# Optimization experiments

Hardware: AMD Instinct MI355X
Metric: run time of the kernel (lower is better)

The kernel has to match this reference:

```python
import jax, jax.numpy as jnp
import numpy as np
from jax import lax

NUM_HEADS = 4
KEY_DEPTHS = 32
ATTN_CH = 32
OUT_CH = 64
IN_CH = 32
KSIZE = 3


def circ_conv3d(x, w, b=None):
    # x: (B,C,D,H,W), w: (O,I,k,k,k); circular padding keeps spatial dims.
    k = w.shape[-1]
    p = k // 2
    if p > 0:
        x = jnp.pad(x, ((0, 0), (0, 0), (p, p), (p, p), (p, p)), mode='wrap')
    y = lax.conv_general_dilated(x, w, (1, 1, 1), 'VALID',
                                 dimension_numbers=('NCDHW', 'OIDHW', 'NCDHW'))
    if b is not None:
        y = y + b[None, :, None, None, None]
    return y


def setup_inputs() -> dict:
    key = jax.random.key(0)
    k1, k2, k3, k4, k5 = jax.random.split(key, 5)
    x = jax.random.normal(k1, (2, IN_CH, 16, 16, 16), dtype=jnp.float32)
    fan = IN_CH * KSIZE ** 3
    w_init = jax.random.normal(k2, (OUT_CH - ATTN_CH, IN_CH, KSIZE, KSIZE, KSIZE), dtype=jnp.float32) / np.sqrt(fan)
    w_qkv = jax.random.normal(k3, (2 * KEY_DEPTHS + ATTN_CH, IN_CH, KSIZE, KSIZE, KSIZE), dtype=jnp.float32) / np.sqrt(fan)
    w_out = jax.random.normal(k4, (ATTN_CH, ATTN_CH, 1, 1, 1), dtype=jnp.float32) / np.sqrt(ATTN_CH)
    b_out = jax.random.normal(k5, (ATTN_CH,), dtype=jnp.float32) * 0.01
    return {'x': x, 'w_init': w_init, 'w_qkv': w_qkv, 'w_out': w_out, 'b_out': b_out}


def reference(x, w_init, w_qkv, w_out, b_out):
    out = circ_conv3d(x, w_init)                      # (b, out-attn, w,h,d)
    b, _, w, h, d = out.shape
    qkv = circ_conv3d(x, w_qkv)                       # (b, 2dk+dv, w,h,d)
    q, k, v = jnp.split(qkv, [KEY_DEPTHS, 2 * KEY_DEPTHS], axis=1)
    dk_h = KEY_DEPTHS // NUM_HEADS
    dv_h = ATTN_CH // NUM_HEADS
    N = w * h * d
    scale = dk_h ** -0.5
    fq = q.reshape(b, NUM_HEADS, dk_h, N) * scale     # (b,H,dk_h,N)
    fk = k.reshape(b, NUM_HEADS, dk_h, N)
    fv = v.reshape(b, NUM_HEADS, dv_h, N)
    logits = jnp.einsum('bhcn,bhcm->bhnm', fq, fk)    # (b,H,N,N)
    weights = jax.nn.softmax(logits, axis=-1)
    attn = jnp.einsum('bhnm,bhvm->bhnv', weights, fv)  # (b,H,N,dv_h)
    # Faithful to torch: a pure reshape (memory reinterpretation), not a transpose.
    attn = attn.reshape(b, NUM_HEADS, dv_h, w, h, d)
    attn = attn.reshape(b, NUM_HEADS * dv_h, w, h, d)  # combine heads
    attn = circ_conv3d(attn, w_out, b_out)             # 1x1x1 conv
    return jnp.concatenate([out, attn], axis=1)
```

## Files before the change

### kernel.cpp

```cpp
#include <hip/hip_runtime.h>


typedef short short8 __attribute__((ext_vector_type(8)));
typedef float float4v __attribute__((ext_vector_type(4)));
typedef unsigned short ushort_t;
typedef unsigned int uint_t;

__device__ inline ushort_t f2bf(float x) {
  uint_t u = __builtin_bit_cast(uint_t, x);
  u += 0x7FFFu + ((u >> 16) & 1u);
  return (ushort_t)(u >> 16);
}

__device__ inline uint_t cvtpk(float lo, float hi) {
  uint_t r;
  asm("v_cvt_pk_bf16_f32 %0, %1, %2" : "=v"(r) : "v"(lo), "v"(hi));
  return r;
}

__global__ __launch_bounds__(256) void kPrep(const float* __restrict__ w_init,
                                             const float* __restrict__ w_qkv,
                                             const float* __restrict__ x,
                                             ushort_t* __restrict__ wA,
                                             ushort_t* __restrict__ xb) {
  __shared__ float xsf[256 * 34];
  int t = threadIdx.x;
  int bx = blockIdx.x;
  if (bx < 432) {
    int idx = bx * 256 + t;
    int j = idx & 7;
    int lane = (idx >> 3) & 63;
    int tap = (idx >> 9) % 27;
    int otile = idx / (27 * 512);
    int o = otile * 16 + (lane & 15);
    int ic = (lane >> 4) * 8 + j;
    const float QS = 0.35355339059327373f * 1.4426950408889634f;
    float v;
    if (o < 32) v = w_init[(o * 32 + ic) * 27 + tap];
    else        v = w_qkv[((o - 32) * 32 + ic) * 27 + tap];
    if (o >= 32 && o < 64) v *= QS;
    wA[idx] = f2bf(v);
  } else {
    int bxx = bx - 432;
    int z = bxx & 15, b = bxx >> 4;
#pragma unroll
    for (int ic = 0; ic < 32; ++ic)
      xsf[t * 34 + ic] = x[((size_t)(b * 32 + ic) * 16 + z) * 256 + t];
    __syncthreads();
#pragma unroll
    for (int r = 0; r < 4; ++r) {
      int slot = r * 256 + t;
      int s = slot >> 2;
      int icg = slot & 3;
      ushort_t tmp[8];
#pragma unroll
      for (int jj = 0; jj < 8; ++jj) tmp[jj] = f2bf(xsf[s * 34 + icg * 8 + jj]);
      *(short8*)(xb + ((size_t)(b * 16 + z) * 256 + s) * 32 + icg * 8) = *(short8*)tmp;
    }
  }
}

__global__ __launch_bounds__(256, 1) void kConv(const ushort_t* __restrict__ xb,
                                                const ushort_t* __restrict__ wA,
                                                float* __restrict__ out,
                                                ushort_t* __restrict__ Qbf,
                                                ushort_t* __restrict__ Kbf,
                                                ushort_t* __restrict__ VtTp) {
  __shared__ ushort_t xs[3 * 256 * 32];
  int tid = threadIdx.x;
  int w = tid >> 6, lane = tid & 63;
  int quad = lane >> 4, nl = lane & 15;
  int bx = blockIdx.x;
  int oq = bx & 3;
  int z = (bx >> 2) & 15;
  int b = bx >> 6;

#pragma unroll
  for (int j = 0; j < 12; ++j) {
    int idx = j * 256 + tid;
    int p = idx >> 10;
    int rem = idx & 1023;
    int zr = (z + p + 15) & 15;
    *(short8*)(xs + p * 8192 + rem * 8) =
        *(const short8*)(xb + (size_t)(b * 16 + zr) * 8192 + rem * 8);
  }
  __syncthreads();

  float4v acc[2][4];
#pragma unroll
  for (int ot = 0; ot < 2; ++ot)
#pragma unroll
    for (int st = 0; st < 4; ++st) acc[ot][st] = (float4v){0.f, 0.f, 0.f, 0.f};

  int y0 = w * 4;
  for (int tap = 0; tap < 27; ++tap) {
    int kz = tap / 9, kyx = tap % 9;
    int ky = kyx / 3, kx = kyx % 3;
    short8 afrag[2];
#pragma unroll
    for (int ot = 0; ot < 2; ++ot)
      afrag[ot] = *(const short8*)(wA + ((size_t)((oq * 2 + ot) * 27 + tap) * 64 + lane) * 8);
    int xsh = (nl + kx + 15) & 15;
#pragma unroll
    for (int st = 0; st < 4; ++st) {
      int yy = (y0 + st + ky + 15) & 15;
      short8 bfrag = *(const short8*)(xs + ((kz * 256) + yy * 16 + xsh) * 32 + quad * 8);
#pragma unroll
      for (int ot = 0; ot < 2; ++ot)
        acc[ot][st] = __builtin_amdgcn_mfma_f32_16x16x32_bf16(afrag[ot], bfrag, acc[ot][st], 0, 0, 0);
    }
  }

#pragma unroll
  for (int st = 0; st < 4; ++st) {
    int y = y0 + st;
    int s = z * 256 + y * 16 + nl;
    int mperm = 2 * nl + (y & 1);
#pragma unroll
    for (int ot = 0; ot < 2; ++ot) {
      int otg = oq * 2 + ot;
#pragma unroll
      for (int r = 0; r < 4; ++r) {
        float val = acc[ot][st][r];
        int oo = (otg & 1) * 16 + quad * 4 + r;
        if (otg < 2) {
          out[(size_t)(b * 64 + oo) * 4096 + s] = val;
        } else if (otg < 4) {
          int h = oo >> 3, c = oo & 7;
          Qbf[((size_t)(b * 4 + h) * 4096 + s) * 8 + c] = f2bf(val);
        } else if (otg < 6) {
          int h = oo >> 3, c = oo & 7;
          Kbf[((size_t)(b * 4 + h) * 4096 + s) * 8 + c] = f2bf(val);
        } else {
          int h = oo >> 3, c = oo & 7;
          VtTp[((size_t)(b * 4 + h) * 8 + c) * 4096 + (size_t)(s & ~31) + mperm] = f2bf(val);
        }
      }
    }
  }
}

__global__ __launch_bounds__(256) void kAttn(const ushort_t* __restrict__ Qbf,
                                             const ushort_t* __restrict__ Kbf,
                                             const ushort_t* __restrict__ VtTp,
                                             float* __restrict__ pacc,
                                             float* __restrict__ pl) {
  __shared__ ushort_t Plds[4 * 2 * 16 * 40];
  int tid = threadIdx.x;
  int w = tid >> 6, lane = tid & 63;
  int id = blockIdx.x * 4 + w;
  int bh = id >> 10;
  int ksp = (id >> 8) & 3;
  int ntile = id & 255;
  int n0 = ntile * 16;
  int quad = lane >> 4, nl = lane & 15;
  int v = nl;

  short8 aq = {};
  if (quad == 0) aq = *(const short8*)(Qbf + ((size_t)bh * 4096 + n0 + nl) * 8);

  short8 ones8;
#pragma unroll
  for (int i = 0; i < 8; ++i) ones8[i] = (short)0x3F80;

  const ushort_t* Krows = Kbf + ((size_t)bh * 4096 + ksp * 1024) * 8;
  const ushort_t* Vbase = VtTp + ((size_t)bh * 8 + (v < 8 ? v : 0)) * 4096
                          + ksp * 1024 + quad * 8;
  ushort_t* Pw = Plds + w * 2 * 640;
  uint_t* Pw32 = (uint_t*)Pw;

  float4v acc = {};

#define QKEXP(mi)                                                              \
  {                                                                            \
    int m0 = (mi) * 32;                                                        \
    short8 bk0 = {}, bk1 = {};                                                 \
    if (quad == 0) {                                                           \
      bk0 = *(const short8*)(Krows + (size_t)(m0 + nl) * 8);                   \
      bk1 = *(const short8*)(Krows + (size_t)(m0 + 16 + nl) * 8);              \
    }                                                                          \
    float4v s0 = __builtin_amdgcn_mfma_f32_16x16x32_bf16(                      \
        aq, bk0, (float4v){0.f, 0.f, 0.f, 0.f}, 0, 0, 0);                      \
    float4v s1 = __builtin_amdgcn_mfma_f32_16x16x32_bf16(                      \
        aq, bk1, (float4v){0.f, 0.f, 0.f, 0.f}, 0, 0, 0);                      \
    uint_t* Pt32 = Pw32 + ((mi) & 1) * 320;                                    \
    _Pragma("unroll") for (int r = 0; r < 4; ++r) {                            \
      float e0 = __builtin_amdgcn_exp2f(s0[r]);                                \
      float e1 = __builtin_amdgcn_exp2f(s1[r]);                                \
      Pt32[(quad * 4 + r) * 20 + nl] = cvtpk(e0, e1);                          \
    }                                                                          \
  }

#define PV(mi)                                                                 \
  {                                                                            \
    const ushort_t* Pt = Pw + ((mi) & 1) * 640;                                \
    short8 a2 = *(const short8*)(Pt + nl * 40 + quad * 8);                     \
    short8 b2;                                                                 \
    if (v < 8)       b2 = *(const short8*)(Vbase + (mi) * 32);                 \
    else if (v == 8) b2 = ones8;                                               \
    else             b2 = (short8){};                                          \
    acc = __builtin_amdgcn_mfma_f32_16x16x32_bf16(a2, b2, acc, 0, 0, 0);       \
  }

  QKEXP(0)
#pragma unroll 2
  for (int mi = 1; mi < 32; ++mi) {
    QKEXP(mi)
    PV(mi - 1)
  }
  PV(31)
#undef QKEXP
#undef PV

#pragma unroll
  for (int r = 0; r < 4; ++r) {
    int rowg = bh * 4096 + n0 + quad * 4 + r;
    if (v < 8)       pacc[((size_t)rowg * 4 + ksp) * 8 + v] = acc[r];
    else if (v == 8) pl[(size_t)rowg * 4 + ksp] = acc[r];
  }
}

__global__ __launch_bounds__(256) void kMerge(const float* __restrict__ pacc,
                                              const float* __restrict__ pl,
                                              float* __restrict__ attn) {
  int idx = blockIdx.x * 256 + threadIdx.x;
  int row = idx >> 3;
  int c = idx & 7;
  float l = 0.f, a = 0.f;
#pragma unroll
  for (int s = 0; s < 4; ++s) {
    l += pl[(size_t)row * 4 + s];
    a += pacc[((size_t)row * 4 + s) * 8 + c];
  }
  int b = row >> 14;
  int h = (row >> 12) & 3;
  int n = row & 4095;
  attn[((size_t)(b * 32 + h * 8 + (n >> 9)) << 12) + ((n & 511) * 8 + c)] = a / l;
}

__global__ __launch_bounds__(256) void kOut(const float* __restrict__ attn,
                                            const float* __restrict__ w_out,
                                            const float* __restrict__ b_out,
                                            float* __restrict__ out) {
  int idx = blockIdx.x * 256 + threadIdx.x;
  int s = idx & 4095;
  int b = (idx >> 12) & 1;
  int cp = idx >> 13;
  float a[32];
#pragma unroll
  for (int ci = 0; ci < 32; ++ci) a[ci] = attn[(size_t)(b * 32 + ci) * 4096 + s];
#pragma unroll
  for (int oo = 0; oo < 2; ++oo) {
    int co = cp * 2 + oo;
    float r = b_out[co];
#pragma unroll
    for (int ci = 0; ci < 32; ++ci) r = fmaf(w_out[co * 32 + ci], a[ci], r);
    out[(size_t)(b * 64 + 32 + co) * 4096 + s] = r;
  }
}

extern "C" void kernel_launch(void* const* d_in, const int* in_sizes, int n_in,
                              void* d_out, int out_size, void* d_ws, size_t ws_size,
                              hipStream_t stream) {
  const float* x      = (const float*)d_in[0];
  const float* w_init = (const float*)d_in[1];
  const float* w_qkv  = (const float*)d_in[2];
  const float* w_out  = (const float*)d_in[3];
  const float* b_out  = (const float*)d_in[4];
  float* out = (float*)d_out;

  ushort_t* wA  = (ushort_t*)d_ws;
  ushort_t* xb  = wA + 110592;
  ushort_t* Qbf = xb + 262144;
  ushort_t* Kbf = Qbf + 262144;
  ushort_t* VtTp = Kbf + 262144;
  float* attn = (float*)(VtTp + 262144);
  float* pacc = attn + 262144;
  float* pl = pacc + 1048576;

  kPrep <<<464,  256, 0, stream>>>(w_init, w_qkv, x, wA, xb);
  kConv <<<128,  256, 0, stream>>>(xb, wA, out, Qbf, Kbf, VtTp);
  kAttn <<<2048, 256, 0, stream>>>(Qbf, Kbf, VtTp, pacc, pl);
  kMerge<<<1024, 256, 0, stream>>>(pacc, pl, attn);
  kOut  <<<512,  256, 0, stream>>>(attn, w_out, b_out, out);
}
```

Before: 124.0 us.

## Process two query tiles per wave in attention, sharing K and V loads

Each wave now handles 32 query rows (two 16-row tiles) instead of 16, so every loaded K block and V block serves both tiles and the grid is halved. The K operand is loaded by all 32 lanes, with the query placed in quad 0 or quad 1 to select the key half, and the next K block is prefetched a step ahead. This cuts redundant global K/V traffic and per-wave overhead. In exchange it uses more registers and LDS per wave and launches half as many waves, which can reduce occupancy and latency hiding.

```diff
diff --git a/kernel.cpp b/kernel.cpp
--- a/kernel.cpp
+++ b/kernel.cpp
@@ -145,78 +145,103 @@
                                              const ushort_t* __restrict__ VtTp,
                                              float* __restrict__ pacc,
                                              float* __restrict__ pl) {
-  __shared__ ushort_t Plds[4 * 2 * 16 * 40];
+  __shared__ ushort_t Plds[4 * 2 * 2 * 640];
   int tid = threadIdx.x;
   int w = tid >> 6, lane = tid & 63;
   int id = blockIdx.x * 4 + w;
-  int bh = id >> 10;
-  int ksp = (id >> 8) & 3;
-  int ntile = id & 255;
-  int n0 = ntile * 16;
+  int bh = id >> 9;
+  int ksp = (id >> 7) & 3;
+  int ntile = id & 127;
+  int n0 = ntile * 32;
   int quad = lane >> 4, nl = lane & 15;
+  int l31 = lane & 31;
   int v = nl;
 
-  short8 aq = {};
-  if (quad == 0) aq = *(const short8*)(Qbf + ((size_t)bh * 4096 + n0 + nl) * 8);
+  short8 z8 = {};
+  short8 q0f = *(const short8*)(Qbf + ((size_t)bh * 4096 + n0 + nl) * 8);
+  short8 q1f = *(const short8*)(Qbf + ((size_t)bh * 4096 + n0 + 16 + nl) * 8);
+  short8 aq0A = (quad == 0) ? q0f : z8;
+  short8 aq0B = (quad == 1) ? q0f : z8;
+  short8 aq1A = (quad == 0) ? q1f : z8;
+  short8 aq1B = (quad == 1) ? q1f : z8;
 
   short8 ones8;
 #pragma unroll
   for (int i = 0; i < 8; ++i) ones8[i] = (short)0x3F80;
 
   const ushort_t* Krows = Kbf + ((size_t)bh * 4096 + ksp * 1024) * 8;
-  const ushort_t* Vbase = VtTp + ((size_t)bh * 8 + (v < 8 ? v : 0)) * 4096
-                          + ksp * 1024 + quad * 8;
-  ushort_t* Pw = Plds + w * 2 * 640;
-  uint_t* Pw32 = (uint_t*)Pw;
-
-  float4v acc = {};
-
-#define QKEXP(mi)                                                              \
+  const ushort_t* Vrow = VtTp + ((size_t)bh * 8 + (v < 8 ? v : 0)) * 4096
+                         + ksp * 1024 + quad * 8;
+  ushort_t* P0 = Plds + (w * 2 + 0) * 2 * 640;
+  ushort_t* P1 = Plds + (w * 2 + 1) * 2 * 640;
+
+  float4v acc0 = {}, acc1 = {};
+
+#define QKEXP(mi, bkr)                                                         \
   {                                                                            \
-    int m0 = (mi) * 32;                                                        \
-    short8 bk0 = {}, bk1 = {};                                                 \
-    if (quad == 0) {                                                           \
-      bk0 = *(const short8*)(Krows + (size_t)(m0 + nl) * 8);                   \
-      bk1 = *(const short8*)(Krows + (size_t)(m0 + 16 + nl) * 8);              \
+    float4v s00 = __builtin_amdgcn_mfma_f32_16x16x32_bf16(                     \
+        aq0A, bkr, (float4v){0.f, 0.f, 0.f, 0.f}, 0, 0, 0);                    \
+    float4v s01 = __builtin_amdgcn_mfma_f32_16x16x32_bf16(                     \
+        aq0B, bkr, (float4v){0.f, 0.f, 0.f, 0.f}, 0, 0, 0);                    \
+    float4v s10 = __builtin_amdgcn_mfma_f32_16x16x32_bf16(                     \
+        aq1A, bkr, (float4v){0.f, 0.f, 0.f, 0.f}, 0, 0, 0);                    \
+    float4v s11 = __builtin_amdgcn_mfma_f32_16x16x32_bf16(                     \
+        aq1B, bkr, (float4v){0.f, 0.f, 0.f, 0.f}, 0, 0, 0);                    \
+    uint_t* Pt0 = (uint_t*)(P0 + ((mi) & 1) * 640);                            \
+    uint_t* Pt1 = (uint_t*)(P1 + ((mi) & 1) * 640);                            \
+    _Pragma("unroll") for (int r = 0; r < 4; ++r) {                            \
+      Pt0[(quad * 4 + r) * 20 + nl] =                                          \
+          cvtpk(__builtin_amdgcn_exp2f(s00[r]), __builtin_amdgcn_exp2f(s01[r]));\
+      Pt1[(quad * 4 + r) * 20 + nl] =                                          \
+          cvtpk(__builtin_amdgcn_exp2f(s10[r]), __builtin_amdgcn_exp2f(s11[r]));\
     }                                                                          \
-    float4v s0 = __builtin_amdgcn_mfma_f32_16x16x32_bf16(                      \
-        aq, bk0, (float4v){0.f, 0.f, 0.f, 0.f}, 0, 0, 0);                      \
-    float4v s1 = __builtin_amdgcn_mfma_f32_16x16x32_bf16(                      \
-        aq, bk1, (float4v){0.f, 0.f, 0.f, 0.f}, 0, 0, 0);                      \
-    uint_t* Pt32 = Pw32 + ((mi) & 1) * 320;                                    \
-    _Pragma("unroll") for (int r = 0; r < 4; ++r) {                            \
-      float e0 = __builtin_amdgcn_exp2f(s0[r]);                                \
-      float e1 = __builtin_amdgcn_exp2f(s1[r]);                                \
-      Pt32[(quad * 4 + r) * 20 + nl] = cvtpk(e0, e1);                          \
-    }                                                                          \
-  }
-
-#define PV(mi)                                                                 \
+  }
+
+#define PVSTEP(a2, bv, accv)                                                   \
   {                                                                            \
-    const ushort_t* Pt = Pw + ((mi) & 1) * 640;                                \
-    short8 a2 = *(const short8*)(Pt + nl * 40 + quad * 8);                     \
-    short8 b2;                                                                 \
-    if (v < 8)       b2 = *(const short8*)(Vbase + (mi) * 32);                 \
-    else if (v == 8) b2 = ones8;                                               \
-    else             b2 = (short8){};                                          \
-    acc = __builtin_amdgcn_mfma_f32_16x16x32_bf16(a2, b2, acc, 0, 0, 0);       \
-  }
-
-  QKEXP(0)
+    short8 b2 = (v < 8) ? (bv) : ((v == 8) ? ones8 : z8);                      \
+    accv = __builtin_amdgcn_mfma_f32_16x16x32_bf16(a2, b2, accv, 0, 0, 0);     \
+  }
+
+  short8 bk = *(const short8*)(Krows + (size_t)l31 * 8);
+  QKEXP(0, bk)
+  bk = *(const short8*)(Krows + (size_t)(32 + l31) * 8);
+
 #pragma unroll 2
   for (int mi = 1; mi < 32; ++mi) {
-    QKEXP(mi)
-    PV(mi - 1)
-  }
-  PV(31)
+    int pb = ((mi - 1) & 1) * 640;
+    short8 a20 = *(const short8*)(P0 + pb + nl * 40 + quad * 8);
+    short8 a21 = *(const short8*)(P1 + pb + nl * 40 + quad * 8);
+    short8 bv = *(const short8*)(Vrow + (mi - 1) * 32);
+    QKEXP(mi, bk)
+    int nxt = ((mi + 1) & 31) * 32;
+    bk = *(const short8*)(Krows + (size_t)(nxt + l31) * 8);
+    PVSTEP(a20, bv, acc0)
+    PVSTEP(a21, bv, acc1)
+  }
+  {
+    int pb = 640;
+    short8 a20 = *(const short8*)(P0 + pb + nl * 40 + quad * 8);
+    short8 a21 = *(const short8*)(P1 + pb + nl * 40 + quad * 8);
+    short8 bv = *(const short8*)(Vrow + 31 * 32);
+    PVSTEP(a20, bv, acc0)
+    PVSTEP(a21, bv, acc1)
+  }
 #undef QKEXP
-#undef PV
+#undef PVSTEP
 
 #pragma unroll
   for (int r = 0; r < 4; ++r) {
-    int rowg = bh * 4096 + n0 + quad * 4 + r;
-    if (v < 8)       pacc[((size_t)rowg * 4 + ksp) * 8 + v] = acc[r];
-    else if (v == 8) pl[(size_t)rowg * 4 + ksp] = acc[r];
+    int rq = quad * 4 + r;
+    int rowg0 = bh * 4096 + n0 + rq;
+    int rowg1 = rowg0 + 16;
+    if (v < 8) {
+      pacc[((size_t)rowg0 * 4 + ksp) * 8 + v] = acc0[r];
+      pacc[((size_t)rowg1 * 4 + ksp) * 8 + v] = acc1[r];
+    } else if (v == 8) {
+      pl[(size_t)rowg0 * 4 + ksp] = acc0[r];
+      pl[(size_t)rowg1 * 4 + ksp] = acc1[r];
+    }
   }
 }
 
@@ -280,7 +305,7 @@
 
   kPrep <<<464,  256, 0, stream>>>(w_init, w_qkv, x, wA, xb);
   kConv <<<128,  256, 0, stream>>>(xb, wA, out, Qbf, Kbf, VtTp);
-  kAttn <<<2048, 256, 0, stream>>>(Qbf, Kbf, VtTp, pacc, pl);
+  kAttn <<<1024, 256, 0, stream>>>(Qbf, Kbf, VtTp, pacc, pl);
   kMerge<<<1024, 256, 0, stream>>>(pacc, pl, attn);
   kOut  <<<512,  256, 0, stream>>>(attn, w_out, b_out, out);
 }
```

After: 109.7 us. 11.6% less time.
